# Kernel optimization log

Measured on AMD Instinct MI355X. Metric: run time of the kernel, lower is better.

## Reference

```python
import jax, jax.numpy as jnp
import numpy as np

NUM_IDS = 8
K_HALF = 5            # k = K//2
DIM = 2048
CP_DIM = DIM // 8     # cp_ratio = 8
N = NUM_IDS * 2 * K_HALF
H, W = 24, 8


def _kaiming(key, out_c, in_c):
    # kaiming_normal_(fan_out, relu) for a 1x1 conv: std = sqrt(2/out_c)
    return jax.random.normal(key, (out_c, in_c), dtype=jnp.float32) * np.sqrt(2.0 / out_c)


def setup_inputs() -> dict:
    key = jax.random.key(0)
    ks = jax.random.split(key, 8)
    inputs = jax.random.normal(ks[0], (N, DIM, H, W), dtype=jnp.float32)
    # PK batch: each identity has K_HALF samples with sub==1 and K_HALF with sub==0
    labels = jnp.repeat(jnp.arange(NUM_IDS, dtype=jnp.int64), 2 * K_HALF)
    sub = jnp.tile(jnp.concatenate([jnp.ones(K_HALF, jnp.int64), jnp.zeros(K_HALF, jnp.int64)]), NUM_IDS)
    return {
        "inputs": inputs,
        "labels": labels,
        "sub": sub,
        "W_ri": _kaiming(ks[1], CP_DIM, DIM),
        "W_rv": _kaiming(ks[2], CP_DIM, DIM),
        "W_ci": _kaiming(ks[3], DIM, K_HALF * CP_DIM),
        "W_cv": _kaiming(ks[4], DIM, K_HALF * CP_DIM),
        "W_f": _kaiming(ks[5], DIM, 2 * DIM),
    }


def reference(inputs, labels, sub, W_ri, W_rv, W_ci, W_cv, W_f):
    n, c, h, w = inputs.shape
    cp = W_ri.shape[0]
    k = W_ci.shape[1] // cp
    n_half = n // 2
    x = jax.lax.stop_gradient(inputs)  # .detach() in the original

    def branch(sub_mask_val, Wr, Wc):
        # indices of samples in this sub-group (order-preserving, like boolean mask)
        sidx = jnp.nonzero(sub == sub_mask_val, size=n_half)[0]
        xs = jnp.einsum('nchw,oc->nohw', x[sidx], Wr)       # [n_half, cp, h, w]
        lab = labels[sidx]                                   # [n_half]
        # for each batch sample, the k positions in the sub-group with matching label
        match = labels[:, None] == lab[None, :]              # [n, n_half]
        pos = jnp.where(match, jnp.arange(n_half)[None, :], n_half)
        gidx = jnp.sort(pos, axis=1)[:, :k]                  # [n, k]
        aff = xs[gidx].reshape(n, k * cp, h, w)              # gather + channel-stack
        return jax.nn.relu(jnp.einsum('nchw,oc->nohw', aff, Wc))

    s_i = branch(1, W_ri, W_ci)   # sub == 1
    s_v = branch(0, W_rv, W_cv)   # sub == 0
    x_fuse = jax.nn.sigmoid(
        jnp.einsum('nchw,oc->nohw', jnp.concatenate([s_i, s_v], axis=1), W_f))
    return inputs + inputs * x_fuse
```

## Files before the change

### kernel.cpp

```cpp
#include <hip/hip_runtime.h>

typedef unsigned short u16;
typedef unsigned int u32;
typedef __bf16 bf16_t;
typedef bf16_t bf16x8 __attribute__((ext_vector_type(8)));
typedef float f32x16 __attribute__((ext_vector_type(16)));

#define DIM 2048
#define HW  192
#define CP  256
#define NB  80

__device__ __forceinline__ u16 f2b(float f) {
    u32 u = __float_as_uint(f);
    u32 r = (u + 0x7FFFu + ((u >> 16) & 1u)) >> 16;
    return (u16)r;
}

__device__ __forceinline__ void g2l16(const void* g, void* l) {
    __builtin_amdgcn_global_load_lds(
        (const __attribute__((address_space(1))) u32*)g,
        (__attribute__((address_space(3))) u32*)l, 16, 0, 0);
}

template<int ACT, bool OUTF32, typename F>
__device__ __forceinline__ void gemm_core(F actAddr, int arstride,
    const u16* __restrict__ Wp, int wstride, int K,
    void* __restrict__ outp, int M)
{
    __shared__ u16 act_s[2][192 * 32];
    __shared__ u16 w_s[2][128 * 32];
    const int t    = threadIdx.x;
    const int wv   = t >> 6;
    const int wn   = wv >> 1;
    const int wm   = wv & 1;
    const int lane = t & 63;
    const int ln   = lane & 31;
    const int q2   = lane >> 5;
    const int swz  = (ln >> 1) & 3;

    f32x16 acc[3][2];
    #pragma unroll
    for (int i = 0; i < 3; ++i)
        #pragma unroll
        for (int j = 0; j < 2; ++j)
            #pragma unroll
            for (int r = 0; r < 16; ++r) acc[i][j][r] = 0.f;

    auto stage = [&](int buf, int k0) {
        const u16* ap = actAddr(k0);
        #pragma unroll
        for (int r = 0; r < 2; ++r) {
            int idx = r * 256 + t;
            int row = idx >> 2, pc = idx & 3;
            int lc  = pc ^ ((row >> 1) & 3);
            g2l16(Wp + (size_t)row * wstride + k0 + lc * 8, (void*)(w_s[buf] + idx * 8));
        }
        #pragma unroll
        for (int r = 0; r < 3; ++r) {
            int idx = r * 256 + t;
            int row = idx >> 2, pc = idx & 3;
            int lc  = pc ^ ((row >> 1) & 3);
            g2l16(ap + (size_t)row * arstride + lc * 8, (void*)(act_s[buf] + idx * 8));
        }
    };

    auto compute = [&](int buf) {
        #pragma unroll
        for (int s = 0; s < 2; ++s) {
            bf16x8 af[3], bf[2];
            const int phys = (s * 2 + q2) ^ swz;
            #pragma unroll
            for (int i = 0; i < 3; ++i)
                af[i] = *(const bf16x8*)(act_s[buf] + ((wn * 96 + i * 32 + ln) * 32 + phys * 8));
            #pragma unroll
            for (int j = 0; j < 2; ++j)
                bf[j] = *(const bf16x8*)(w_s[buf] + ((wm * 64 + j * 32 + ln) * 32 + phys * 8));
            #pragma unroll
            for (int i = 0; i < 3; ++i)
                #pragma unroll
                for (int j = 0; j < 2; ++j)
                    acc[i][j] = __builtin_amdgcn_mfma_f32_32x32x16_bf16(
                        af[i], bf[j], acc[i][j], 0, 0, 0);
        }
    };

    stage(0, 0);
    const int iters = K / 32;
    for (int it = 0; it < iters; ++it) {
        int b = it & 1;
        __syncthreads();
        if (it + 1 < iters) stage(b ^ 1, (it + 1) * 32);
        compute(b);
    }

    #pragma unroll
    for (int i = 0; i < 3; ++i) {
        #pragma unroll
        for (int j = 0; j < 2; ++j) {
            #pragma unroll
            for (int r = 0; r < 16; ++r) {
                float v = acc[i][j][r];
                if (ACT == 1) v = v > 0.f ? v : 0.f;
                int nl = wn * 96 + i * 32 + (r & 3) + 8 * (r >> 2) + 4 * q2;
                int ml = wm * 64 + j * 32 + ln;
                if (OUTF32) ((float*)outp)[(size_t)nl * M + ml] = v;
                else        ((u16*)outp)[(size_t)nl * M + ml] = f2b(v);
            }
        }
    }
}

__global__ __launch_bounds__(256) void proj_g(const u16* __restrict__ xt,
    const int* __restrict__ sub, int nbase,
    const u16* __restrict__ Wri, const u16* __restrict__ Wrv,
    float* __restrict__ proj4)
{
    const int zz = blockIdx.z, z = zz >> 2, p = zz & 3;
    const int bm = blockIdx.x;
    const int n = nbase + z;
    const u16* act = xt + (size_t)z * (HW * DIM) + p * 512;
    const u16* Wp  = ((sub[n] != 0) ? Wri : Wrv) + (size_t)bm * 128 * DIM + p * 512;
    float* outp = proj4 + (size_t)p * ((size_t)NB * HW * CP)
                + (size_t)n * (HW * CP) + bm * 128;
    auto f = [=](int k0) { return act + k0; };
    gemm_core<0, true>(f, DIM, Wp, DIM, 512, outp, CP);
}

__global__ __launch_bounds__(256) void proj_red(const float* __restrict__ proj4,
                                                u16* __restrict__ projt)
{
    const size_t i = ((size_t)blockIdx.x * 256 + threadIdx.x) * 4;
    const size_t S = (size_t)NB * HW * CP;
    float4 a = *(const float4*)(proj4 + i);
    float4 b = *(const float4*)(proj4 + i + S);
    float4 c = *(const float4*)(proj4 + i + 2 * S);
    float4 d = *(const float4*)(proj4 + i + 3 * S);
    ushort4 o;
    o.x = f2b(a.x + b.x + c.x + d.x);
    o.y = f2b(a.y + b.y + c.y + d.y);
    o.z = f2b(a.z + b.z + c.z + d.z);
    o.w = f2b(a.w + b.w + c.w + d.w);
    *(ushort4*)(projt + i) = o;
}

__global__ __launch_bounds__(256) void compose_g(const u16* __restrict__ projt,
    const u16* __restrict__ Wci, const u16* __restrict__ Wcv,
    u16* __restrict__ st)
{
    const int z = blockIdx.z, br = z >> 3, id = z & 7;
    const int bm = blockIdx.x;
    const u16* base = projt + (size_t)(id * 10 + br * 5) * (HW * CP);
    const u16* Wp   = (br ? Wcv : Wci) + (size_t)bm * 128 * 1280;
    u16* outp = st + (size_t)(id * 2 + br) * (HW * DIM) + bm * 128;
    auto f = [=](int k0) { return base + (size_t)(k0 >> 8) * (HW * CP) + (k0 & 255); };
    gemm_core<1, false>(f, CP, Wp, 1280, 1280, outp, DIM);
}

__global__ __launch_bounds__(256) void fuse_g(const u16* __restrict__ st,
    const u16* __restrict__ Wf, float* __restrict__ fuset4)
{
    const int z = blockIdx.z, h = z >> 3, id = z & 7;
    const int bm = blockIdx.x;
    const u16* base = st + (size_t)(id * 2 + (h >> 1)) * (HW * DIM) + (h & 1) * 1024;
    const u16* Wp   = Wf + (size_t)bm * 128 * (2 * DIM) + (size_t)h * 1024;
    float* outp = fuset4 + (size_t)h * (8 * HW * DIM) + (size_t)id * (HW * DIM) + bm * 128;
    auto f = [=](int k0) { return base + k0; };
    gemm_core<0, true>(f, DIM, Wp, 2 * DIM, 1024, outp, DIM);
}

__global__ __launch_bounds__(256) void prep_k(const float* __restrict__ x,
    u16* __restrict__ xt, int nxt, int wc,
    const float* __restrict__ a0, const float* __restrict__ a1,
    const float* __restrict__ a2, const float* __restrict__ a3,
    const float* __restrict__ a4,
    u16* __restrict__ o0, u16* __restrict__ o1, u16* __restrict__ o2,
    u16* __restrict__ o3, u16* __restrict__ o4)
{
    __shared__ float ts[64][65];
    const int b = blockIdx.x;
    const int t = threadIdx.x;
    if (b < nxt) {
        const int z = b / 96, r6 = b % 96;
        const int p0 = (r6 % 3) * 64, c0 = (r6 / 3) * 64;
        #pragma unroll
        for (int r = 0; r < 4; ++r) {
            int idx = r * 256 + t;
            int c = idx >> 4, p4 = (idx & 15) * 4;
            float4 v = *(const float4*)(x + ((size_t)z * DIM + c0 + c) * HW + p0 + p4);
            ts[c][p4 + 0] = v.x; ts[c][p4 + 1] = v.y;
            ts[c][p4 + 2] = v.z; ts[c][p4 + 3] = v.w;
        }
        __syncthreads();
        #pragma unroll
        for (int r = 0; r < 4; ++r) {
            int idx = r * 256 + t;
            int p = idx >> 4, c4 = (idx & 15) * 4;
            ushort4 o;
            o.x = f2b(ts[c4 + 0][p]); o.y = f2b(ts[c4 + 1][p]);
            o.z = f2b(ts[c4 + 2][p]); o.w = f2b(ts[c4 + 3][p]);
            *(ushort4*)(xt + ((size_t)z * HW + p0 + p) * DIM + c0 + c4) = o;
        }
    } else if (wc) {
        size_t off = ((size_t)(b - nxt) * 256 + t) * 4;
        const float* s; u16* d;
        if (off < 524288)                    { s = a0; d = o0; }
        else if ((off -= 524288) < 524288)   { s = a1; d = o1; }
        else if ((off -= 524288) < 2621440)  { s = a2; d = o2; }
        else if ((off -= 2621440) < 2621440) { s = a3; d = o3; }
        else                                 { off -= 2621440; s = a4; d = o4; }
        float4 v = *(const float4*)(s + off);
        ushort4 p;
        p.x = f2b(v.x); p.y = f2b(v.y); p.z = f2b(v.z); p.w = f2b(v.w);
        *(ushort4*)(d + off) = p;
    }
}

__global__ __launch_bounds__(256) void fuse_tr(const float* __restrict__ fuset4,
                                               float* __restrict__ fuse)
{
    __shared__ float ts[64][65];
    const int id = blockIdx.z;
    const int c0 = blockIdx.x * 64, p0 = blockIdx.y * 64;
    const int t = threadIdx.x, l = t & 63;
    const size_t hs = (size_t)8 * HW * DIM;
    #pragma unroll
    for (int i = 0; i < 16; ++i) {
        int pl = (t >> 6) * 16 + i;
        size_t a = ((size_t)id * HW + p0 + pl) * DIM + c0 + l;
        float v = fuset4[a] + fuset4[a + hs] + fuset4[a + 2 * hs] + fuset4[a + 3 * hs];
        ts[pl][l] = 1.f / (1.f + __expf(-v));
    }
    __syncthreads();
    #pragma unroll
    for (int i = 0; i < 16; ++i) {
        int cl = (t >> 6) * 16 + i;
        fuse[((size_t)id * DIM + c0 + cl) * HW + p0 + l] = ts[l][cl];
    }
}

__global__ __launch_bounds__(256) void final_kernel(const float* __restrict__ x,
    const int* __restrict__ labels, const float* __restrict__ fusebuf,
    float* __restrict__ out)
{
    const u32 e = ((u32)blockIdx.x * 256u + threadIdx.x) * 4u;
    const u32 n   = e / ((u32)DIM * HW);
    const u32 rem = e % ((u32)DIM * HW);
    const int id  = labels[n];
    float4 xv = *reinterpret_cast<const float4*>(x + e);
    float4 fv = *reinterpret_cast<const float4*>(fusebuf + (size_t)id * DIM * HW + rem);
    float4 o;
    o.x = xv.x + xv.x * fv.x;
    o.y = xv.y + xv.y * fv.y;
    o.z = xv.z + xv.z * fv.z;
    o.w = xv.w + xv.w * fv.w;
    *reinterpret_cast<float4*>(out + e) = o;
}

extern "C" void kernel_launch(void* const* d_in, const int* in_sizes, int n_in,
                              void* d_out, int out_size, void* d_ws, size_t ws_size,
                              hipStream_t stream) {
    const float* x      = (const float*)d_in[0];
    const int*   labels = (const int*)d_in[1];
    const int*   sub    = (const int*)d_in[2];
    const float* Wri    = (const float*)d_in[3];
    const float* Wrv    = (const float*)d_in[4];
    const float* Wci    = (const float*)d_in[5];
    const float* Wcv    = (const float*)d_in[6];
    const float* Wf     = (const float*)d_in[7];
    float* out = (float*)d_out;
    char* ws = (char*)d_ws;

    const bool full = ws_size >= (size_t)175636480;
    const size_t xtb = full ? (size_t)62914560 : (size_t)15728640;

    u16* Wri_b = (u16*)(ws);
    u16* Wrv_b = (u16*)(ws + 1048576);
    u16* Wci_b = (u16*)(ws + 2097152);
    u16* Wcv_b = (u16*)(ws + 7340032);
    u16* Wf_b  = (u16*)(ws + 12582912);
    u16* xtbuf = (u16*)(ws + 29360128);
    u16* projt = (u16*)(ws + 29360128 + xtb);
    u16* stb   = (u16*)(ws + 29360128 + xtb + 7864320);
    float* fuset4 = (float*)(ws + 29360128 + xtb + 7864320 + 12582912);
    float* fuse   = (float*)(ws + 29360128 + xtb + 7864320 + 12582912 + 50331648);
    float* proj4 = fuset4;

    const int nchunk = full ? 1 : 4;
    const int cs = NB / nchunk;
    for (int c = 0; c < nchunk; ++c) {
        const int nxt = 96 * cs;
        const int wc = (c == 0) ? 1 : 0;
        prep_k<<<nxt + (wc ? 14336 : 0), 256, 0, stream>>>(
            x + (size_t)c * cs * DIM * HW, xtbuf, nxt, wc,
            Wri, Wrv, Wci, Wcv, Wf, Wri_b, Wrv_b, Wci_b, Wcv_b, Wf_b);
        proj_g<<<dim3(2, 1, cs * 4), 256, 0, stream>>>(xtbuf, sub, c * cs, Wri_b, Wrv_b, proj4);
    }
    proj_red<<<3840, 256, 0, stream>>>(proj4, projt);
    compose_g<<<dim3(16, 1, 16), 256, 0, stream>>>(projt, Wci_b, Wcv_b, stb);
    fuse_g   <<<dim3(16, 1, 32), 256, 0, stream>>>(stb, Wf_b, fuset4);
    fuse_tr  <<<dim3(32, 3, 8), 256, 0, stream>>>(fuset4, fuse);
    final_kernel<<<30720, 256, 0, stream>>>(x, labels, fuse, out);
}
```

Before: 426.0 us.

## Swizzle GEMM block order across XCDs and widen prep transpose tiles

Remaps the linear block index in the projection, compose and fuse GEMM kernels so that consecutive logical tiles, which share weight or activation rows, are spread across the eight XCDs in contiguous groups. The goal is better L2 locality per XCD. Separately, the input transpose kernel now converts to bf16 before staging in LDS and handles a full 64-channel by 192-pixel tile per block with 16-byte stores. This uses fewer blocks and wider writes, in exchange for a larger LDS footprint and possible LDS bank conflicts on the strided column reads.

New measurement: 428.4 us. Within noise of the previous version (+0.6%).

```diff
diff --git a/kernel.cpp b/kernel.cpp
--- a/kernel.cpp
+++ b/kernel.cpp
@@ -21,6 +21,10 @@
     __builtin_amdgcn_global_load_lds(
         (const __attribute__((address_space(1))) u32*)g,
         (__attribute__((address_space(3))) u32*)l, 16, 0, 0);
+}
+
+__device__ __forceinline__ int xcdswz(int lid, int n) {
+    return (lid & 7) * (n >> 3) + (lid >> 3);
 }
 
 template<int ACT, bool OUTF32, typename F>
@@ -116,8 +120,11 @@
     const u16* __restrict__ Wri, const u16* __restrict__ Wrv,
     float* __restrict__ proj4)
 {
-    const int zz = blockIdx.z, z = zz >> 2, p = zz & 3;
-    const int bm = blockIdx.x;
+    const int nblk = gridDim.x * gridDim.z;
+    const int lid  = blockIdx.x + gridDim.x * blockIdx.z;
+    const int s    = xcdswz(lid, nblk);
+    const int bm = s & 1, zz = s >> 1;
+    const int z = zz >> 2, p = zz & 3;
     const int n = nbase + z;
     const u16* act = xt + (size_t)z * (HW * DIM) + p * 512;
     const u16* Wp  = ((sub[n] != 0) ? Wri : Wrv) + (size_t)bm * 128 * DIM + p * 512;
@@ -148,8 +155,10 @@
     const u16* __restrict__ Wci, const u16* __restrict__ Wcv,
     u16* __restrict__ st)
 {
-    const int z = blockIdx.z, br = z >> 3, id = z & 7;
-    const int bm = blockIdx.x;
+    const int lid = blockIdx.x + 16 * blockIdx.z;
+    const int s   = xcdswz(lid, 256);
+    const int bm = s & 15, z = s >> 4;
+    const int br = z >> 3, id = z & 7;
     const u16* base = projt + (size_t)(id * 10 + br * 5) * (HW * CP);
     const u16* Wp   = (br ? Wcv : Wci) + (size_t)bm * 128 * 1280;
     u16* outp = st + (size_t)(id * 2 + br) * (HW * DIM) + bm * 128;
@@ -160,8 +169,10 @@
 __global__ __launch_bounds__(256) void fuse_g(const u16* __restrict__ st,
     const u16* __restrict__ Wf, float* __restrict__ fuset4)
 {
-    const int z = blockIdx.z, h = z >> 3, id = z & 7;
-    const int bm = blockIdx.x;
+    const int lid = blockIdx.x + 16 * blockIdx.z;
+    const int s   = xcdswz(lid, 512);
+    const int bm = s & 15, z = s >> 4;
+    const int h = z >> 3, id = z & 7;
     const u16* base = st + (size_t)(id * 2 + (h >> 1)) * (HW * DIM) + (h & 1) * 1024;
     const u16* Wp   = Wf + (size_t)bm * 128 * (2 * DIM) + (size_t)h * 1024;
     float* outp = fuset4 + (size_t)h * (8 * HW * DIM) + (size_t)id * (HW * DIM) + bm * 128;
@@ -177,29 +188,33 @@
     u16* __restrict__ o0, u16* __restrict__ o1, u16* __restrict__ o2,
     u16* __restrict__ o3, u16* __restrict__ o4)
 {
-    __shared__ float ts[64][65];
+    __shared__ u16 ts[64][210];
     const int b = blockIdx.x;
     const int t = threadIdx.x;
     if (b < nxt) {
-        const int z = b / 96, r6 = b % 96;
-        const int p0 = (r6 % 3) * 64, c0 = (r6 / 3) * 64;
-        #pragma unroll
-        for (int r = 0; r < 4; ++r) {
-            int idx = r * 256 + t;
-            int c = idx >> 4, p4 = (idx & 15) * 4;
-            float4 v = *(const float4*)(x + ((size_t)z * DIM + c0 + c) * HW + p0 + p4);
-            ts[c][p4 + 0] = v.x; ts[c][p4 + 1] = v.y;
-            ts[c][p4 + 2] = v.z; ts[c][p4 + 3] = v.w;
+        const int z = b >> 5, c0 = (b & 31) * 64;
+        const float* src = x + ((size_t)z * DIM + c0) * HW;
+        #pragma unroll
+        for (int i = 0; i < 12; ++i) {
+            int idx = i * 256 + t;
+            float4 v = *(const float4*)(src + (size_t)idx * 4);
+            int c = idx / 48, p4 = (idx % 48) * 4;
+            u32 lo = ((u32)f2b(v.y) << 16) | f2b(v.x);
+            u32 hi = ((u32)f2b(v.w) << 16) | f2b(v.z);
+            *(u32*)&ts[c][p4]     = lo;
+            *(u32*)&ts[c][p4 + 2] = hi;
         }
         __syncthreads();
         #pragma unroll
-        for (int r = 0; r < 4; ++r) {
-            int idx = r * 256 + t;
-            int p = idx >> 4, c4 = (idx & 15) * 4;
-            ushort4 o;
-            o.x = f2b(ts[c4 + 0][p]); o.y = f2b(ts[c4 + 1][p]);
-            o.z = f2b(ts[c4 + 2][p]); o.w = f2b(ts[c4 + 3][p]);
-            *(ushort4*)(xt + ((size_t)z * HW + p0 + p) * DIM + c0 + c4) = o;
+        for (int i = 0; i < 6; ++i) {
+            int u = i * 256 + t;
+            int c8 = (u & 7) * 8, p = u >> 3;
+            u32 w0 = ((u32)ts[c8 + 1][p] << 16) | ts[c8 + 0][p];
+            u32 w1 = ((u32)ts[c8 + 3][p] << 16) | ts[c8 + 2][p];
+            u32 w2 = ((u32)ts[c8 + 5][p] << 16) | ts[c8 + 4][p];
+            u32 w3 = ((u32)ts[c8 + 7][p] << 16) | ts[c8 + 6][p];
+            uint4 o4v; o4v.x = w0; o4v.y = w1; o4v.z = w2; o4v.w = w3;
+            *(uint4*)(xt + ((size_t)z * HW + p) * DIM + c0 + c8) = o4v;
         }
     } else if (wc) {
         size_t off = ((size_t)(b - nxt) * 256 + t) * 4;
@@ -289,7 +304,7 @@
     const int nchunk = full ? 1 : 4;
     const int cs = NB / nchunk;
     for (int c = 0; c < nchunk; ++c) {
-        const int nxt = 96 * cs;
+        const int nxt = 32 * cs;
         const int wc = (c == 0) ? 1 : 0;
         prep_k<<<nxt + (wc ? 14336 : 0), 256, 0, stream>>>(
             x + (size_t)c * cs * DIM * HW, xtbuf, nxt, wc,
```
